# Kernel tuning notes

Hardware: AMD Instinct MI355X
Metric: run time of the kernel (lower is better)

Reference implementation:

```python
import jax, jax.numpy as jnp
import numpy as np

GROUPS = 32
EPS = 1e-5


def setup_inputs() -> dict:
    key = jax.random.key(0)
    k1, k2, k3, k4, k5 = jax.random.split(key, 5)
    B, C, H, W = 16, 256, 80, 80
    cg = C // GROUPS  # 8 channels per group
    x = jax.random.normal(k1, (B, C, H, W), dtype=jnp.float32)
    # conv1x1: Conv2d(cg, cg, 1) -> weight [cg, cg], bias [cg]
    fan_in = cg
    bound = 1.0 / np.sqrt(fan_in)
    conv_w = jax.random.uniform(k2, (cg, cg), minval=-bound, maxval=bound, dtype=jnp.float32)
    conv_b = jax.random.uniform(k3, (cg,), minval=-bound, maxval=bound, dtype=jnp.float32)
    # GroupNorm(num_groups=cg, num_channels=cg) affine params (init: ones/zeros)
    gn_w = jnp.ones((cg,), dtype=jnp.float32)
    gn_b = jnp.zeros((cg,), dtype=jnp.float32)
    return {"x": x, "conv_w": conv_w, "conv_b": conv_b, "gn_w": gn_w, "gn_b": gn_b}


def reference(x, conv_w, conv_b, gn_w, gn_b):
    b, c, h, w = x.shape
    cg = c // GROUPS
    gx = x.reshape(b * GROUPS, cg, h, w)  # [bg, cg, h, w]

    def norm(t):
        # GroupNorm with num_groups == num_channels: per-channel norm over (h, w)
        mu = jnp.mean(t, axis=(2, 3), keepdims=True)
        var = jnp.var(t, axis=(2, 3), keepdims=True)
        tn = (t - mu) * jax.lax.rsqrt(var + EPS)
        return tn * gn_w[None, :, None, None] + gn_b[None, :, None, None]

    def gate_branch(ph, pw):
        # ph: [bg, cg, h] (pooled over w), pw: [bg, cg, w] (pooled over h)
        cat = jnp.concatenate([ph, pw], axis=2)  # [bg, cg, h+w]
        hw = jnp.einsum('bcl,oc->bol', cat, conv_w) + conv_b[None, :, None]
        gh, gw = hw[:, :, :h], hw[:, :, h:]
        gated = gx * jax.nn.sigmoid(gh)[..., None] * jax.nn.sigmoid(gw)[:, :, None, :]
        return norm(gated)

    # avg-pool branch
    x1 = gate_branch(jnp.mean(gx, axis=3), jnp.mean(gx, axis=2))
    # max-pool branch
    y1 = gate_branch(jnp.max(gx, axis=3), jnp.max(gx, axis=2))

    x11 = x1.reshape(b * GROUPS, cg, h * w)
    y11 = y1.reshape(b * GROUPS, cg, h * w)
    # channel-attention vectors: softmax over the cg channel axis
    x12 = jax.nn.softmax(jnp.mean(x1, axis=(2, 3)), axis=-1)  # [bg, cg]  (avg pool)
    y12 = jax.nn.softmax(jnp.max(y1, axis=(2, 3)), axis=-1)   # [bg, cg]  (max pool)

    weights = jnp.einsum('bc,bcl->bl', x12, y11) + jnp.einsum('bc,bcl->bl', y12, x11)
    weights = weights.reshape(b * GROUPS, 1, h, w)
    return (gx * jax.nn.sigmoid(weights)).reshape(b, c, h, w)
```

## Files before the change

kernel.cpp:

```cpp
#include <hip/hip_runtime.h>
#include <math.h>

constexpr int CG = 8;
constexpr int HW = 6400;
constexpr int NG = 512;
constexpr float EPSf = 1e-5f;

__device__ __forceinline__ float sigmoidf(float v) {
    return 1.0f / (1.0f + __expf(-v));
}

__global__ __launch_bounds__(512, 4) void k_fused(
    const float* __restrict__ x,
    const float* __restrict__ conv_w,
    const float* __restrict__ conv_b,
    const float* __restrict__ gnw,
    const float* __restrict__ gnb,
    float* __restrict__ out)
{
    const int bg  = blockIdx.x;
    const int tid = threadIdx.x;

    __shared__ float tile[80 * 84];
    __shared__ float pools[4 * 640];
    __shared__ float g[4 * 640];
    __shared__ float wsm[64];
    __shared__ float cbs[8];
    __shared__ float stats[8][8];
    __shared__ float Axs[8], Bxs[8], Ays[8], Bys[8], ymaxs[8], cHx[8], cHy[8];
    __shared__ float kcs;

    if (tid < 64) wsm[tid] = conv_w[tid];
    if (tid < 8)  cbs[tid] = conv_b[tid];

    const float* base = x + (size_t)bg * CG * HW;

    for (int c = 0; c < 8; ++c) {
        __syncthreads();
        for (int i = 0; i < 4; ++i) {
            const int v = tid + i * 512;
            if (v < 1600) {
                float4 d = ((const float4*)(base + c * HW))[v];
                const int h = v / 20, w0 = (v % 20) * 4;
                *(float4*)&tile[h * 84 + w0] = d;
            }
        }
        __syncthreads();
        if (tid < 320) {
            const int r = tid >> 2, q = tid & 3;
            float s = 0.f, m = -INFINITY;
            const float4* rp = (const float4*)&tile[r * 84];
            #pragma unroll
            for (int k = q * 5; k < q * 5 + 5; ++k) {
                float4 d = rp[k];
                s += d.x + d.y + d.z + d.w;
                m = fmaxf(m, fmaxf(fmaxf(d.x, d.y), fmaxf(d.z, d.w)));
            }
            s += __shfl_down(s, 2, 4); s += __shfl_down(s, 1, 4);
            m = fmaxf(m, __shfl_down(m, 2, 4));
            m = fmaxf(m, __shfl_down(m, 1, 4));
            if (q == 0) {
                pools[0 * 640 + c * 80 + r] = s * (1.f / 80.f);
                pools[2 * 640 + c * 80 + r] = m;
            }
            float s2 = 0.f, m2 = -INFINITY;
            #pragma unroll 4
            for (int hh = q * 20; hh < q * 20 + 20; ++hh) {
                const float vv = tile[hh * 84 + r];
                s2 += vv;
                m2 = fmaxf(m2, vv);
            }
            s2 += __shfl_down(s2, 2, 4); s2 += __shfl_down(s2, 1, 4);
            m2 = fmaxf(m2, __shfl_down(m2, 2, 4));
            m2 = fmaxf(m2, __shfl_down(m2, 1, 4));
            if (q == 0) {
                pools[1 * 640 + c * 80 + r] = s2 * (1.f / 80.f);
                pools[3 * 640 + c * 80 + r] = m2;
            }
        }
    }
    __syncthreads();

    for (int i = 0; i < 5; ++i) {
        const int e = tid + i * 512;
        if (e < 2560) {
            const int a = e / 640, rem = e % 640, c = rem / 80, p = rem % 80;
            float acc = cbs[c];
            #pragma unroll
            for (int cc = 0; cc < 8; ++cc)
                acc += wsm[c * 8 + cc] * pools[a * 640 + cc * 80 + p];
            g[e] = sigmoidf(acc);
        }
    }
    __syncthreads();

    {
        const int c = tid >> 6, lane = tid & 63;
        const float* cb_ = base + c * HW;
        float s1x = 0.f, s2x = 0.f, s1y = 0.f, s2y = 0.f;
        float my = -INFINITY, ny = INFINITY;
        for (int j = 0; j < 25; ++j) {
            const int v = lane + j * 64;
            float4 d = ((const float4*)cb_)[v];
            const int h = v / 20, w0 = (v % 20) * 4;
            const float ghx = g[0 * 640 + c * 80 + h];
            const float ghy = g[2 * 640 + c * 80 + h];
            const float4 gwx = *(const float4*)&g[1 * 640 + c * 80 + w0];
            const float4 gwy = *(const float4*)&g[3 * 640 + c * 80 + w0];
            const float dd[4]  = {d.x, d.y, d.z, d.w};
            const float gx4[4] = {gwx.x, gwx.y, gwx.z, gwx.w};
            const float gy4[4] = {gwy.x, gwy.y, gwy.z, gwy.w};
            #pragma unroll
            for (int k = 0; k < 4; ++k) {
                const float tx = dd[k] * ghx * gx4[k];
                const float ty = dd[k] * ghy * gy4[k];
                s1x += tx; s2x += tx * tx;
                s1y += ty; s2y += ty * ty;
                my = fmaxf(my, ty); ny = fminf(ny, ty);
            }
        }
        #pragma unroll
        for (int off = 32; off > 0; off >>= 1) {
            s1x += __shfl_down(s1x, off);
            s2x += __shfl_down(s2x, off);
            s1y += __shfl_down(s1y, off);
            s2y += __shfl_down(s2y, off);
            my = fmaxf(my, __shfl_down(my, off));
            ny = fminf(ny, __shfl_down(ny, off));
        }
        if (lane == 0) {
            stats[c][0] = s1x; stats[c][1] = s2x; stats[c][2] = s1y;
            stats[c][3] = s2y; stats[c][4] = my;  stats[c][5] = ny;
        }
    }
    __syncthreads();

    if (tid < 8) {
        const float s1x = stats[tid][0], s2x = stats[tid][1];
        const float s1y = stats[tid][2], s2y = stats[tid][3];
        const float my  = stats[tid][4], ny  = stats[tid][5];
        const float w = gnw[tid], b = gnb[tid];
        const float mux  = s1x * (1.f / 6400.f);
        const float varx = s2x * (1.f / 6400.f) - mux * mux;
        const float ax   = rsqrtf(varx + EPSf) * w;
        Axs[tid] = ax; Bxs[tid] = b - mux * ax;
        const float muy  = s1y * (1.f / 6400.f);
        const float vary = s2y * (1.f / 6400.f) - muy * muy;
        const float ay   = rsqrtf(vary + EPSf) * w;
        Ays[tid] = ay; Bys[tid] = b - muy * ay;
        ymaxs[tid] = (ay >= 0.f ? my : ny) * ay + Bys[tid];
    }
    __syncthreads();
    if (tid == 0) {
        float x12[8], y12[8];
        float mb = -INFINITY;
        for (int c = 0; c < 8; ++c) mb = fmaxf(mb, gnb[c]);
        float se = 0.f;
        for (int c = 0; c < 8; ++c) { x12[c] = __expf(gnb[c] - mb); se += x12[c]; }
        float inv = 1.f / se;
        for (int c = 0; c < 8; ++c) x12[c] *= inv;
        float m2 = -INFINITY;
        for (int c = 0; c < 8; ++c) m2 = fmaxf(m2, ymaxs[c]);
        se = 0.f;
        for (int c = 0; c < 8; ++c) { y12[c] = __expf(ymaxs[c] - m2); se += y12[c]; }
        inv = 1.f / se;
        float kc = 0.f;
        for (int c = 0; c < 8; ++c) {
            y12[c] *= inv;
            cHx[c] = y12[c] * Axs[c];
            cHy[c] = x12[c] * Ays[c];
            kc += x12[c] * Bys[c] + y12[c] * Bxs[c];
        }
        kcs = kc;
    }
    __syncthreads();
    for (int i = 0; i < 3; ++i) {
        const int e = tid + i * 512;
        if (e < 1280) {
            if (e < 640) g[e]                 *= cHx[e / 80];
            else         g[1280 + (e - 640)]  *= cHy[(e - 640) / 80];
        }
    }
    __syncthreads();

    const float kc = kcs;
    float* ob = out + (size_t)bg * CG * HW;
    for (int i = 0; i < 4; ++i) {
        const int v = tid + i * 512;
        if (v < 1600) {
            const int h = v / 20, w0 = (v % 20) * 4;
            float4 gxv[8];
            #pragma unroll
            for (int c = 0; c < 8; ++c)
                gxv[c] = *(const float4*)(base + c * HW + v * 4);

            float s0 = kc, s1 = kc, s2 = kc, s3 = kc;
            #pragma unroll
            for (int c = 0; c < 8; ++c) {
                const float chx = g[0 * 640 + c * 80 + h];
                const float chy = g[2 * 640 + c * 80 + h];
                const float4 cwx = *(const float4*)&g[1 * 640 + c * 80 + w0];
                const float4 cwy = *(const float4*)&g[3 * 640 + c * 80 + w0];
                s0 += gxv[c].x * (chy * cwy.x + chx * cwx.x);
                s1 += gxv[c].y * (chy * cwy.y + chx * cwx.y);
                s2 += gxv[c].z * (chy * cwy.z + chx * cwx.z);
                s3 += gxv[c].w * (chy * cwy.w + chx * cwx.w);
            }
            s0 = sigmoidf(s0); s1 = sigmoidf(s1);
            s2 = sigmoidf(s2); s3 = sigmoidf(s3);
            #pragma unroll
            for (int c = 0; c < 8; ++c) {
                float4 o;
                o.x = gxv[c].x * s0; o.y = gxv[c].y * s1;
                o.z = gxv[c].z * s2; o.w = gxv[c].w * s3;
                *(float4*)(ob + c * HW + v * 4) = o;
            }
        }
    }
}

extern "C" void kernel_launch(void* const* d_in, const int* in_sizes, int n_in,
                              void* d_out, int out_size, void* d_ws, size_t ws_size,
                              hipStream_t stream) {
    const float* x      = (const float*)d_in[0];
    const float* conv_w = (const float*)d_in[1];
    const float* conv_b = (const float*)d_in[2];
    const float* gn_w   = (const float*)d_in[3];
    const float* gn_b   = (const float*)d_in[4];
    float* out = (float*)d_out;
    (void)d_ws; (void)ws_size;

    k_fused<<<NG, 512, 0, stream>>>(x, conv_w, conv_b, gn_w, gn_b, out);
}
```

Before: 69.80 us.

## Split fused kernel into pool, mid-stats, and output kernels for more parallelism

```diff
diff --git a/kernel.cpp b/kernel.cpp
--- a/kernel.cpp
+++ b/kernel.cpp
@@ -1,94 +1,99 @@
 #include <hip/hip_runtime.h>
 #include <math.h>
 
-constexpr int CG = 8;
-constexpr int HW = 6400;
-constexpr int NG = 512;
+constexpr int CG   = 8;
+constexpr int Hh   = 80;
+constexpr int HW   = 6400;
+constexpr int NG   = 512;
+constexpr int NCH  = NG * CG;
+constexpr int PP   = NCH * 80;
 constexpr float EPSf = 1e-5f;
+
+constexpr int COEF = 4 * PP;
 
 __device__ __forceinline__ float sigmoidf(float v) {
     return 1.0f / (1.0f + __expf(-v));
 }
 
-__global__ __launch_bounds__(512, 4) void k_fused(
-    const float* __restrict__ x,
-    const float* __restrict__ conv_w,
-    const float* __restrict__ conv_b,
-    const float* __restrict__ gnw,
-    const float* __restrict__ gnb,
-    float* __restrict__ out)
-{
+__global__ __launch_bounds__(256) void k_pool(const float* __restrict__ x,
+                                              float* __restrict__ ws) {
+    const int bgc = blockIdx.x;
+    const float* base = x + (size_t)bgc * HW;
+    __shared__ float tile[Hh * 84];
+
+    for (int v = threadIdx.x; v < 1600; v += 256) {
+        int h  = v / 20;
+        int w0 = (v % 20) * 4;
+        float4 d = ((const float4*)base)[v];
+        *(float4*)&tile[h * 84 + w0] = d;
+    }
+    __syncthreads();
+
+    const int t = threadIdx.x;
+    if (t < 80) {
+        float s = 0.f, m = -INFINITY;
+        const float4* r = (const float4*)&tile[t * 84];
+        #pragma unroll
+        for (int i = 0; i < 20; i++) {
+            float4 d = r[i];
+            s += d.x + d.y + d.z + d.w;
+            m = fmaxf(m, fmaxf(fmaxf(d.x, d.y), fmaxf(d.z, d.w)));
+        }
+        ws[0 * PP + bgc * 80 + t] = s * (1.f / 80.f);
+        ws[2 * PP + bgc * 80 + t] = m;
+    } else if (t >= 128 && t < 208) {
+        const int c = t - 128;
+        float s2 = 0.f, m2 = -INFINITY;
+        #pragma unroll 8
+        for (int i = 0; i < 80; i++) {
+            float v = tile[i * 84 + c];
+            s2 += v;
+            m2 = fmaxf(m2, v);
+        }
+        ws[1 * PP + bgc * 80 + c] = s2 * (1.f / 80.f);
+        ws[3 * PP + bgc * 80 + c] = m2;
+    }
+}
+
+__global__ __launch_bounds__(512) void k_mid(const float* __restrict__ x,
+                                             const float* __restrict__ conv_w,
+                                             const float* __restrict__ conv_b,
+                                             const float* __restrict__ gnw,
+                                             const float* __restrict__ gnb,
+                                             float* __restrict__ ws) {
     const int bg  = blockIdx.x;
     const int tid = threadIdx.x;
 
-    __shared__ float tile[80 * 84];
-    __shared__ float pools[4 * 640];
+    __shared__ float pl[4 * 640];
     __shared__ float g[4 * 640];
     __shared__ float wsm[64];
     __shared__ float cbs[8];
-    __shared__ float stats[8][8];
+    __shared__ float stats[8][6];
     __shared__ float Axs[8], Bxs[8], Ays[8], Bys[8], ymaxs[8], cHx[8], cHy[8];
     __shared__ float kcs;
 
     if (tid < 64) wsm[tid] = conv_w[tid];
     if (tid < 8)  cbs[tid] = conv_b[tid];
 
-    const float* base = x + (size_t)bg * CG * HW;
-
-    for (int c = 0; c < 8; ++c) {
-        __syncthreads();
-        for (int i = 0; i < 4; ++i) {
-            const int v = tid + i * 512;
-            if (v < 1600) {
-                float4 d = ((const float4*)(base + c * HW))[v];
-                const int h = v / 20, w0 = (v % 20) * 4;
-                *(float4*)&tile[h * 84 + w0] = d;
-            }
-        }
-        __syncthreads();
-        if (tid < 320) {
-            const int r = tid >> 2, q = tid & 3;
-            float s = 0.f, m = -INFINITY;
-            const float4* rp = (const float4*)&tile[r * 84];
-            #pragma unroll
-            for (int k = q * 5; k < q * 5 + 5; ++k) {
-                float4 d = rp[k];
-                s += d.x + d.y + d.z + d.w;
-                m = fmaxf(m, fmaxf(fmaxf(d.x, d.y), fmaxf(d.z, d.w)));
-            }
-            s += __shfl_down(s, 2, 4); s += __shfl_down(s, 1, 4);
-            m = fmaxf(m, __shfl_down(m, 2, 4));
-            m = fmaxf(m, __shfl_down(m, 1, 4));
-            if (q == 0) {
-                pools[0 * 640 + c * 80 + r] = s * (1.f / 80.f);
-                pools[2 * 640 + c * 80 + r] = m;
-            }
-            float s2 = 0.f, m2 = -INFINITY;
-            #pragma unroll 4
-            for (int hh = q * 20; hh < q * 20 + 20; ++hh) {
-                const float vv = tile[hh * 84 + r];
-                s2 += vv;
-                m2 = fmaxf(m2, vv);
-            }
-            s2 += __shfl_down(s2, 2, 4); s2 += __shfl_down(s2, 1, 4);
-            m2 = fmaxf(m2, __shfl_down(m2, 2, 4));
-            m2 = fmaxf(m2, __shfl_down(m2, 1, 4));
-            if (q == 0) {
-                pools[1 * 640 + c * 80 + r] = s2 * (1.f / 80.f);
-                pools[3 * 640 + c * 80 + r] = m2;
-            }
-        }
-    }
-    __syncthreads();
-
+    #pragma unroll
     for (int i = 0; i < 5; ++i) {
         const int e = tid + i * 512;
         if (e < 2560) {
             const int a = e / 640, rem = e % 640, c = rem / 80, p = rem % 80;
+            pl[e] = ws[a * PP + (bg * 8 + c) * 80 + p];
+        }
+    }
+    __syncthreads();
+
+    #pragma unroll
+    for (int i = 0; i < 5; ++i) {
+        const int e = tid + i * 512;
+        if (e < 2560) {
+            const int rem = e % 640, a = e / 640, c = rem / 80, p = rem % 80;
             float acc = cbs[c];
             #pragma unroll
             for (int cc = 0; cc < 8; ++cc)
-                acc += wsm[c * 8 + cc] * pools[a * 640 + cc * 80 + p];
+                acc += wsm[c * 8 + cc] * pl[a * 640 + cc * 80 + p];
             g[e] = sigmoidf(acc);
         }
     }
@@ -96,7 +101,7 @@
 
     {
         const int c = tid >> 6, lane = tid & 63;
-        const float* cb_ = base + c * HW;
+        const float* cb_ = x + (size_t)(bg * 8 + c) * HW;
         float s1x = 0.f, s2x = 0.f, s1y = 0.f, s2y = 0.f;
         float my = -INFINITY, ny = INFINITY;
         for (int j = 0; j < 25; ++j) {
@@ -174,20 +179,47 @@
         kcs = kc;
     }
     __syncthreads();
-    for (int i = 0; i < 3; ++i) {
+    for (int e = tid; e < 640; e += 512) {
+        g[e]        *= cHx[e / 80];
+        g[1280 + e] *= cHy[e / 80];
+    }
+    __syncthreads();
+
+    float* cf = ws + COEF + (size_t)bg * 2568;
+    #pragma unroll
+    for (int i = 0; i < 5; ++i) {
         const int e = tid + i * 512;
-        if (e < 1280) {
-            if (e < 640) g[e]                 *= cHx[e / 80];
-            else         g[1280 + (e - 640)]  *= cHy[(e - 640) / 80];
-        }
-    }
+        if (e < 2560) cf[e] = g[e];
+    }
+    if (tid == 0) cf[2560] = kcs;
+}
+
+__global__ __launch_bounds__(256) void k_out(const float* __restrict__ x,
+                                             const float* __restrict__ ws,
+                                             float* __restrict__ out) {
+    const int bg = blockIdx.x >> 2;
+    const int q  = blockIdx.x & 3;
+    const int tid = threadIdx.x;
+
+    __shared__ float g[2560];
+    __shared__ float kcs;
+    const float* cf = ws + COEF + (size_t)bg * 2568;
+    #pragma unroll
+    for (int i = 0; i < 10; ++i) {
+        const int e = tid + i * 256;
+        if (e < 2560) g[e] = cf[e];
+    }
+    if (tid == 0) kcs = cf[2560];
     __syncthreads();
 
     const float kc = kcs;
-    float* ob = out + (size_t)bg * CG * HW;
-    for (int i = 0; i < 4; ++i) {
-        const int v = tid + i * 512;
-        if (v < 1600) {
+    const float* base = x + (size_t)bg * CG * HW;
+    float*       ob   = out + (size_t)bg * CG * HW;
+
+    #pragma unroll
+    for (int i = 0; i < 2; ++i) {
+        const int v = q * 400 + tid + i * 256;
+        if (v < (q + 1) * 400) {
             const int h = v / 20, w0 = (v % 20) * 4;
             float4 gxv[8];
             #pragma unroll
@@ -228,7 +260,9 @@
     const float* gn_w   = (const float*)d_in[3];
     const float* gn_b   = (const float*)d_in[4];
     float* out = (float*)d_out;
-    (void)d_ws; (void)ws_size;
-
-    k_fused<<<NG, 512, 0, stream>>>(x, conv_w, conv_b, gn_w, gn_b, out);
-}
+    float* ws  = (float*)d_ws;
+
+    k_pool<<<NCH,    256, 0, stream>>>(x, ws);
+    k_mid <<<NG,     512, 0, stream>>>(x, conv_w, conv_b, gn_w, gn_b, ws);
+    k_out <<<NG * 4, 256, 0, stream>>>(x, ws, out);
+}
```

Result: slower. 79.27 us (+13.6%).

## Double-buffer channel tiles and double block size to 1024 threads

Applied to the files above, without the earlier changes.

```diff
diff --git a/kernel.cpp b/kernel.cpp
--- a/kernel.cpp
+++ b/kernel.cpp
@@ -1,16 +1,17 @@
 #include <hip/hip_runtime.h>
 #include <math.h>
 
-constexpr int CG = 8;
-constexpr int HW = 6400;
-constexpr int NG = 512;
+constexpr int CG  = 8;
+constexpr int HW  = 6400;
+constexpr int NG  = 512;
+constexpr int TSF = 88;
 constexpr float EPSf = 1e-5f;
 
 __device__ __forceinline__ float sigmoidf(float v) {
     return 1.0f / (1.0f + __expf(-v));
 }
 
-__global__ __launch_bounds__(512, 4) void k_fused(
+__global__ __launch_bounds__(1024, 8) void k_fused(
     const float* __restrict__ x,
     const float* __restrict__ conv_w,
     const float* __restrict__ conv_b,
@@ -21,12 +22,12 @@
     const int bg  = blockIdx.x;
     const int tid = threadIdx.x;
 
-    __shared__ float tile[80 * 84];
+    __shared__ float tl[2][80 * TSF];
     __shared__ float pools[4 * 640];
     __shared__ float g[4 * 640];
     __shared__ float wsm[64];
     __shared__ float cbs[8];
-    __shared__ float stats[8][8];
+    __shared__ float red[16][6];
     __shared__ float Axs[8], Bxs[8], Ays[8], Bys[8], ymaxs[8], cHx[8], cHy[8];
     __shared__ float kcs;
 
@@ -35,25 +36,34 @@
 
     const float* base = x + (size_t)bg * CG * HW;
 
+    {
+        const float4 p0 = ((const float4*)base)[tid];
+        float4 p1;
+        if (tid < 576) p1 = ((const float4*)base)[1024 + tid];
+        *(float4*)&tl[0][(tid / 20) * TSF + (tid % 20) * 4] = p0;
+        if (tid < 576) {
+            const int v = 1024 + tid;
+            *(float4*)&tl[0][(v / 20) * TSF + (v % 20) * 4] = p1;
+        }
+    }
+    __syncthreads();
+
     for (int c = 0; c < 8; ++c) {
-        __syncthreads();
-        for (int i = 0; i < 4; ++i) {
-            const int v = tid + i * 512;
-            if (v < 1600) {
-                float4 d = ((const float4*)(base + c * HW))[v];
-                const int h = v / 20, w0 = (v % 20) * 4;
-                *(float4*)&tile[h * 84 + w0] = d;
-            }
-        }
-        __syncthreads();
+        const int cur = c & 1;
+        float4 p0, p1;
+        if (c < 7) {
+            const float* cb = base + (c + 1) * HW;
+            p0 = ((const float4*)cb)[tid];
+            if (tid < 576) p1 = ((const float4*)cb)[1024 + tid];
+        }
         if (tid < 320) {
             const int r = tid >> 2, q = tid & 3;
+            const float4* rp = (const float4*)&tl[cur][r * TSF];
             float s = 0.f, m = -INFINITY;
-            const float4* rp = (const float4*)&tile[r * 84];
             #pragma unroll
             for (int k = q * 5; k < q * 5 + 5; ++k) {
                 float4 d = rp[k];
-                s += d.x + d.y + d.z + d.w;
+                s += (d.x + d.y) + (d.z + d.w);
                 m = fmaxf(m, fmaxf(fmaxf(d.x, d.y), fmaxf(d.z, d.w)));
             }
             s += __shfl_down(s, 2, 4); s += __shfl_down(s, 1, 4);
@@ -63,26 +73,37 @@
                 pools[0 * 640 + c * 80 + r] = s * (1.f / 80.f);
                 pools[2 * 640 + c * 80 + r] = m;
             }
-            float s2 = 0.f, m2 = -INFINITY;
-            #pragma unroll 4
+        } else if (tid >= 512 && tid < 832) {
+            const int e = tid - 512, j = e >> 2, q = e & 3;
+            float s = 0.f, m = -INFINITY;
+            #pragma unroll 5
             for (int hh = q * 20; hh < q * 20 + 20; ++hh) {
-                const float vv = tile[hh * 84 + r];
-                s2 += vv;
-                m2 = fmaxf(m2, vv);
-            }
-            s2 += __shfl_down(s2, 2, 4); s2 += __shfl_down(s2, 1, 4);
-            m2 = fmaxf(m2, __shfl_down(m2, 2, 4));
-            m2 = fmaxf(m2, __shfl_down(m2, 1, 4));
+                const float vv = tl[cur][hh * TSF + j];
+                s += vv;
+                m = fmaxf(m, vv);
+            }
+            s += __shfl_down(s, 2, 4); s += __shfl_down(s, 1, 4);
+            m = fmaxf(m, __shfl_down(m, 2, 4));
+            m = fmaxf(m, __shfl_down(m, 1, 4));
             if (q == 0) {
-                pools[1 * 640 + c * 80 + r] = s2 * (1.f / 80.f);
-                pools[3 * 640 + c * 80 + r] = m2;
-            }
-        }
-    }
-    __syncthreads();
-
-    for (int i = 0; i < 5; ++i) {
-        const int e = tid + i * 512;
+                pools[1 * 640 + c * 80 + j] = s * (1.f / 80.f);
+                pools[3 * 640 + c * 80 + j] = m;
+            }
+        }
+        if (c < 7) {
+            float* nx = tl[cur ^ 1];
+            *(float4*)&nx[(tid / 20) * TSF + (tid % 20) * 4] = p0;
+            if (tid < 576) {
+                const int v = 1024 + tid;
+                *(float4*)&nx[(v / 20) * TSF + (v % 20) * 4] = p1;
+            }
+        }
+        __syncthreads();
+    }
+
+    #pragma unroll
+    for (int i = 0; i < 3; ++i) {
+        const int e = tid + i * 1024;
         if (e < 2560) {
             const int a = e / 640, rem = e % 640, c = rem / 80, p = rem % 80;
             float acc = cbs[c];
@@ -95,28 +116,31 @@
     __syncthreads();
 
     {
-        const int c = tid >> 6, lane = tid & 63;
+        const int c = tid >> 7, sl = tid & 127;
         const float* cb_ = base + c * HW;
         float s1x = 0.f, s2x = 0.f, s1y = 0.f, s2y = 0.f;
         float my = -INFINITY, ny = INFINITY;
-        for (int j = 0; j < 25; ++j) {
-            const int v = lane + j * 64;
-            float4 d = ((const float4*)cb_)[v];
-            const int h = v / 20, w0 = (v % 20) * 4;
-            const float ghx = g[0 * 640 + c * 80 + h];
-            const float ghy = g[2 * 640 + c * 80 + h];
-            const float4 gwx = *(const float4*)&g[1 * 640 + c * 80 + w0];
-            const float4 gwy = *(const float4*)&g[3 * 640 + c * 80 + w0];
-            const float dd[4]  = {d.x, d.y, d.z, d.w};
-            const float gx4[4] = {gwx.x, gwx.y, gwx.z, gwx.w};
-            const float gy4[4] = {gwy.x, gwy.y, gwy.z, gwy.w};
-            #pragma unroll
-            for (int k = 0; k < 4; ++k) {
-                const float tx = dd[k] * ghx * gx4[k];
-                const float ty = dd[k] * ghy * gy4[k];
-                s1x += tx; s2x += tx * tx;
-                s1y += ty; s2y += ty * ty;
-                my = fmaxf(my, ty); ny = fminf(ny, ty);
+        #pragma unroll 4
+        for (int j = 0; j < 13; ++j) {
+            const int v = sl + j * 128;
+            if (v < 1600) {
+                float4 d = ((const float4*)cb_)[v];
+                const int h = v / 20, w0 = (v % 20) * 4;
+                const float ghx = g[0 * 640 + c * 80 + h];
+                const float ghy = g[2 * 640 + c * 80 + h];
+                const float4 gwx = *(const float4*)&g[1 * 640 + c * 80 + w0];
+                const float4 gwy = *(const float4*)&g[3 * 640 + c * 80 + w0];
+                const float dd[4]  = {d.x, d.y, d.z, d.w};
+                const float gx4[4] = {gwx.x, gwx.y, gwx.z, gwx.w};
+                const float gy4[4] = {gwy.x, gwy.y, gwy.z, gwy.w};
+                #pragma unroll
+                for (int k = 0; k < 4; ++k) {
+                    const float tx = dd[k] * ghx * gx4[k];
+                    const float ty = dd[k] * ghy * gy4[k];
+                    s1x += tx; s2x += tx * tx;
+                    s1y += ty; s2y += ty * ty;
+                    my = fmaxf(my, ty); ny = fminf(ny, ty);
+                }
             }
         }
         #pragma unroll
@@ -128,17 +152,21 @@
             my = fmaxf(my, __shfl_down(my, off));
             ny = fminf(ny, __shfl_down(ny, off));
         }
-        if (lane == 0) {
-            stats[c][0] = s1x; stats[c][1] = s2x; stats[c][2] = s1y;
-            stats[c][3] = s2y; stats[c][4] = my;  stats[c][5] = ny;
+        const int wv = tid >> 6;
+        if ((tid & 63) == 0) {
+            red[wv][0] = s1x; red[wv][1] = s2x; red[wv][2] = s1y;
+            red[wv][3] = s2y; red[wv][4] = my;  red[wv][5] = ny;
         }
     }
     __syncthreads();
 
     if (tid < 8) {
-        const float s1x = stats[tid][0], s2x = stats[tid][1];
-        const float s1y = stats[tid][2], s2y = stats[tid][3];
-        const float my  = stats[tid][4], ny  = stats[tid][5];
+        const float s1x = red[2 * tid][0] + red[2 * tid + 1][0];
+        const float s2x = red[2 * tid][1] + red[2 * tid + 1][1];
+        const float s1y = red[2 * tid][2] + red[2 * tid + 1][2];
+        const float s2y = red[2 * tid][3] + red[2 * tid + 1][3];
+        const float my  = fmaxf(red[2 * tid][4], red[2 * tid + 1][4]);
+        const float ny  = fminf(red[2 * tid][5], red[2 * tid + 1][5]);
         const float w = gnw[tid], b = gnb[tid];
         const float mux  = s1x * (1.f / 6400.f);
         const float varx = s2x * (1.f / 6400.f) - mux * mux;
@@ -174,19 +202,17 @@
         kcs = kc;
     }
     __syncthreads();
-    for (int i = 0; i < 3; ++i) {
-        const int e = tid + i * 512;
-        if (e < 1280) {
-            if (e < 640) g[e]                 *= cHx[e / 80];
-            else         g[1280 + (e - 640)]  *= cHy[(e - 640) / 80];
-        }
+    if (tid < 640) {
+        g[tid]        *= cHx[tid / 80];
+        g[1280 + tid] *= cHy[tid / 80];
     }
     __syncthreads();
 
     const float kc = kcs;
     float* ob = out + (size_t)bg * CG * HW;
-    for (int i = 0; i < 4; ++i) {
-        const int v = tid + i * 512;
+    #pragma unroll
+    for (int i = 0; i < 2; ++i) {
+        const int v = tid + i * 1024;
         if (v < 1600) {
             const int h = v / 20, w0 = (v % 20) * 4;
             float4 gxv[8];
@@ -198,9 +224,9 @@
             #pragma unroll
             for (int c = 0; c < 8; ++c) {
                 const float chx = g[0 * 640 + c * 80 + h];
-                const float chy = g[2 * 640 + c * 80 + h];
-                const float4 cwx = *(const float4*)&g[1 * 640 + c * 80 + w0];
-                const float4 cwy = *(const float4*)&g[3 * 640 + c * 80 + w0];
+                const float chy = g[1280 + c * 80 + h];
+                const float4 cwx = *(const float4*)&g[640  + c * 80 + w0];
+                const float4 cwy = *(const float4*)&g[1920 + c * 80 + w0];
                 s0 += gxv[c].x * (chy * cwy.x + chx * cwx.x);
                 s1 += gxv[c].y * (chy * cwy.y + chx * cwx.y);
                 s2 += gxv[c].z * (chy * cwy.z + chx * cwx.z);
@@ -230,5 +256,5 @@
     float* out = (float*)d_out;
     (void)d_ws; (void)ws_size;
 
-    k_fused<<<NG, 512, 0, stream>>>(x, conv_w, conv_b, gn_w, gn_b, out);
+    k_fused<<<NG, 1024, 0, stream>>>(x, conv_w, conv_b, gn_w, gn_b, out);
 }
```

Measured after the change: 106.7 us. +52.8%, slower.
